# Kernel optimization log

Hardware: AMD Instinct MI355X
Metric: run time of the kernel (lower is better)

Reference implementation:

```python
import jax, jax.numpy as jnp
import numpy as np

K0 = 16                       # partial-sum length used for the t-test
TAU = -2.053748910631823      # threshold from the kernel (negative -> test never passes)


def setup_inputs() -> dict:
    key = jax.random.key(0)
    kx, kw = jax.random.split(key)
    B, S, DIN, DOUT = 4, 2048, 4096, 4096
    x = jax.random.normal(kx, (B, S, DIN), dtype=jnp.float32)
    W = jax.random.normal(kw, (DOUT, DIN), dtype=jnp.float32) * 0.02
    return {"x": x, "W": W}


def reference(x, W):
    # Faithful translation of linear_etu_kernel (including its quirks):
    #  - phase 1: partial dot over first K0=16 features -> y1, s2
    #  - t-test: passed = |y1|/sqrt(s2/K0) < TAU (TAU<0 so always False)
    #  - phase 2: loops k in [K0, DOUT) but the loads omit the n/m offsets,
    #    so it accumulates a scalar c = sum_k W[0,k]*x_row0[k] into every
    #    still-active output. Bias is never read by the kernel.
    orig_shape = x.shape
    DOUT = W.shape[0]
    x2 = x.reshape(-1, orig_shape[-1])            # [N, DIN]
    xk = x2[:, :K0]                               # [N, K0]
    wk = W[:, :K0]                                # [DOUT, K0]
    y1 = xk @ wk.T                                # [N, DOUT]
    s2 = (xk * xk) @ (wk * wk).T                  # [N, DOUT] sum of prod^2
    tstat = jnp.abs(y1) / jnp.sqrt(s2 / K0)
    passed = tstat < TAU                          # always False (kept faithful)
    active = (~passed).astype(y1.dtype)
    # phase-2 quirk: uses W row 0 and x row 0 only, k in [K0, DOUT)
    c = jnp.sum(W[0, K0:DOUT] * x2[0, K0:DOUT])   # scalar
    acc = y1 + c * active
    out = jnp.where(passed, jnp.float32(0.0), acc)
    return out.reshape(*orig_shape[:-1], DOUT)
```

## Files before the change

### kernel.cpp

```cpp
#include <hip/hip_runtime.h>

constexpr int K0   = 16;
constexpr int DIN  = 4096;
constexpr int DOUT = 4096;

constexpr int BLOCK           = 256;
constexpr int COLS_PER_THREAD = 4;
constexpr int COLS_PER_BLOCK  = BLOCK * COLS_PER_THREAD;
constexpr int ROWS_PER_BLOCK  = 32;

__global__ __launch_bounds__(256) void c_reduce(const float* __restrict__ x,
                                                const float* __restrict__ W,
                                                float* __restrict__ c_out) {
    __shared__ float lds[4];
    const int tid = threadIdx.x;
    float acc = 0.0f;
    for (int t = K0 + tid; t < DOUT; t += 256)
        acc = fmaf(W[t], x[t], acc);
    #pragma unroll
    for (int off = 32; off > 0; off >>= 1)
        acc += __shfl_down(acc, off, 64);
    if ((tid & 63) == 0) lds[tid >> 6] = acc;
    __syncthreads();
    if (tid == 0)
        *c_out = lds[0] + lds[1] + lds[2] + lds[3];
}

__global__ __launch_bounds__(BLOCK) void et_row(const float* __restrict__ x,
                                                const float* __restrict__ W,
                                                const float* __restrict__ c_ptr,
                                                float* __restrict__ out) {
    const int tid  = threadIdx.x;
    const int j0   = blockIdx.x * COLS_PER_BLOCK + tid * COLS_PER_THREAD;
    const int row0 = blockIdx.y * ROWS_PER_BLOCK;

    float wk[COLS_PER_THREAD][K0];
    #pragma unroll
    for (int cc = 0; cc < COLS_PER_THREAD; ++cc) {
        const float4* wp = (const float4*)(W + (size_t)(j0 + cc) * DIN);
        #pragma unroll
        for (int q = 0; q < K0 / 4; ++q) {
            float4 v = wp[q];
            wk[cc][4 * q + 0] = v.x;
            wk[cc][4 * q + 1] = v.y;
            wk[cc][4 * q + 2] = v.z;
            wk[cc][4 * q + 3] = v.w;
        }
    }

    const float c = *c_ptr;

    for (int r = 0; r < ROWS_PER_BLOCK; ++r) {
        const int row = row0 + r;
        const float* xr = x + (size_t)row * DIN;

        float xk[K0];
        #pragma unroll
        for (int q = 0; q < K0 / 4; ++q) {
            float4 v = ((const float4*)xr)[q];
            xk[4 * q + 0] = v.x;
            xk[4 * q + 1] = v.y;
            xk[4 * q + 2] = v.z;
            xk[4 * q + 3] = v.w;
        }

        float acc[COLS_PER_THREAD];
        #pragma unroll
        for (int cc = 0; cc < COLS_PER_THREAD; ++cc) {
            float s = c;
            #pragma unroll
            for (int k = 0; k < K0; ++k)
                s = fmaf(xk[k], wk[cc][k], s);
            acc[cc] = s;
        }

        float4 o = make_float4(acc[0], acc[1], acc[2], acc[3]);
        *((float4*)(out + (size_t)row * DOUT + j0)) = o;
    }
}

extern "C" void kernel_launch(void* const* d_in, const int* in_sizes, int n_in,
                              void* d_out, int out_size, void* d_ws, size_t ws_size,
                              hipStream_t stream) {
    const float* x  = (const float*)d_in[0];
    const float* W  = (const float*)d_in[1];
    float* out      = (float*)d_out;
    float* c_ws     = (float*)d_ws;

    const int nrows = in_sizes[0] / DIN;

    c_reduce<<<1, 256, 0, stream>>>(x, W, c_ws);

    dim3 grid(DOUT / COLS_PER_BLOCK, nrows / ROWS_PER_BLOCK);
    et_row<<<grid, BLOCK, 0, stream>>>(x, W, c_ws, out);
}
```

Measured before the change: 264.2 us.

## Fuse scalar reduction into main kernel and use nontemporal output stores

Removes the separate single-block c_reduce launch and has every block recompute the scalar dot product of W row 0 and x row 0 redundantly, then broadcast it through LDS. This drops one kernel launch and the serial dependency between the two kernels. In exchange each block now does about 4K extra loads, which should hit in cache. Output writes switch to nontemporal vector stores to avoid polluting cache, and the row loop is unrolled by two.

```diff
diff --git a/kernel.cpp b/kernel.cpp
--- a/kernel.cpp
+++ b/kernel.cpp
@@ -9,27 +9,13 @@
 constexpr int COLS_PER_BLOCK  = BLOCK * COLS_PER_THREAD;
 constexpr int ROWS_PER_BLOCK  = 32;
 
-__global__ __launch_bounds__(256) void c_reduce(const float* __restrict__ x,
-                                                const float* __restrict__ W,
-                                                float* __restrict__ c_out) {
-    __shared__ float lds[4];
-    const int tid = threadIdx.x;
-    float acc = 0.0f;
-    for (int t = K0 + tid; t < DOUT; t += 256)
-        acc = fmaf(W[t], x[t], acc);
-    #pragma unroll
-    for (int off = 32; off > 0; off >>= 1)
-        acc += __shfl_down(acc, off, 64);
-    if ((tid & 63) == 0) lds[tid >> 6] = acc;
-    __syncthreads();
-    if (tid == 0)
-        *c_out = lds[0] + lds[1] + lds[2] + lds[3];
-}
+typedef float vfloat4 __attribute__((ext_vector_type(4)));
 
-__global__ __launch_bounds__(BLOCK) void et_row(const float* __restrict__ x,
-                                                const float* __restrict__ W,
-                                                const float* __restrict__ c_ptr,
-                                                float* __restrict__ out) {
+__global__ __launch_bounds__(BLOCK) void et_fused(const float* __restrict__ x,
+                                                  const float* __restrict__ W,
+                                                  float* __restrict__ out) {
+    __shared__ float lds_c[4];
+    __shared__ float c_sh;
     const int tid  = threadIdx.x;
     const int j0   = blockIdx.x * COLS_PER_BLOCK + tid * COLS_PER_THREAD;
     const int row0 = blockIdx.y * ROWS_PER_BLOCK;
@@ -48,8 +34,19 @@
         }
     }
 
-    const float c = *c_ptr;
+    float acc = 0.0f;
+    for (int t = K0 + tid; t < DIN; t += BLOCK)
+        acc = fmaf(W[t], x[t], acc);
+    #pragma unroll
+    for (int off = 32; off > 0; off >>= 1)
+        acc += __shfl_down(acc, off, 64);
+    if ((tid & 63) == 0) lds_c[tid >> 6] = acc;
+    __syncthreads();
+    if (tid == 0) c_sh = lds_c[0] + lds_c[1] + lds_c[2] + lds_c[3];
+    __syncthreads();
+    const float c = c_sh;
 
+    #pragma unroll 2
     for (int r = 0; r < ROWS_PER_BLOCK; ++r) {
         const int row = row0 + r;
         const float* xr = x + (size_t)row * DIN;
@@ -64,33 +61,28 @@
             xk[4 * q + 3] = v.w;
         }
 
-        float acc[COLS_PER_THREAD];
+        vfloat4 o;
         #pragma unroll
         for (int cc = 0; cc < COLS_PER_THREAD; ++cc) {
             float s = c;
             #pragma unroll
             for (int k = 0; k < K0; ++k)
                 s = fmaf(xk[k], wk[cc][k], s);
-            acc[cc] = s;
+            o[cc] = s;
         }
-
-        float4 o = make_float4(acc[0], acc[1], acc[2], acc[3]);
-        *((float4*)(out + (size_t)row * DOUT + j0)) = o;
+        __builtin_nontemporal_store(o, (vfloat4*)(out + (size_t)row * DOUT + j0));
     }
 }
 
 extern "C" void kernel_launch(void* const* d_in, const int* in_sizes, int n_in,
                               void* d_out, int out_size, void* d_ws, size_t ws_size,
                               hipStream_t stream) {
-    const float* x  = (const float*)d_in[0];
-    const float* W  = (const float*)d_in[1];
-    float* out      = (float*)d_out;
-    float* c_ws     = (float*)d_ws;
+    const float* x = (const float*)d_in[0];
+    const float* W = (const float*)d_in[1];
+    float* out     = (float*)d_out;
 
     const int nrows = in_sizes[0] / DIN;
 
-    c_reduce<<<1, 256, 0, stream>>>(x, W, c_ws);
-
     dim3 grid(DOUT / COLS_PER_BLOCK, nrows / ROWS_PER_BLOCK);
-    et_row<<<grid, BLOCK, 0, stream>>>(x, W, c_ws, out);
+    et_fused<<<grid, BLOCK, 0, stream>>>(x, W, out);
 }
```

Result: faster. 244.3 us (-7.5%).
